# Kernel optimization log

Measured on AMD Instinct MI355X. Metric: run time of the kernel, lower is better.

The kernel has to match this reference:

```python
import jax, jax.numpy as jnp
import numpy as np

A_DIM = 6
VBR = jnp.array([300.0, 750.0, 1200.0, 1850.0, 2850.0, 4300.0])
MAX_BR = 4300.0
BUF = 30000.0  # buffer_size fixed to 30000 each forward
N_STEPS = 6    # unrolled iterations in the source (cooked_bw[0]..cooked_bw[5])


def _conv_feat(x, w, b):
    # 1-channel valid Conv1d(kernel=4) + ReLU, flattened channel-major like torch .view
    L = x.shape[0]
    idx = jnp.arange(L - 3)[:, None] + jnp.arange(4)[None, :]
    win = x[idx]                                   # (L-3, 4)
    out = jax.nn.relu(win @ w[:, 0, :].T + b)      # (L-3, 128)
    return out.T.reshape(-1)                       # (128*(L-3),)


def setup_inputs() -> dict:
    key = jax.random.key(0)
    ks = jax.random.split(key, 12)
    s = 0.1
    return {
        "inp": jax.random.uniform(ks[0], (8, 8), jnp.float32) + 0.1,
        "conv_w": jax.random.normal(ks[1], (128, 1, 4), jnp.float32) * s,
        "conv_b": jax.random.normal(ks[2], (128,), jnp.float32) * s,
        "w0": jax.random.normal(ks[3], (128, 1), jnp.float32) * s,
        "b0": jax.random.normal(ks[4], (128,), jnp.float32) * s,
        "w1": jax.random.normal(ks[5], (128, 1), jnp.float32) * s,
        "b1": jax.random.normal(ks[6], (128,), jnp.float32) * s,
        "w2": jax.random.normal(ks[7], (128, 1), jnp.float32) * s,
        "b2": jax.random.normal(ks[8], (128,), jnp.float32) * s,
        "w3": jax.random.normal(ks[9], (128, 2048), jnp.float32) * 0.02,
        "b3": jax.random.normal(ks[10], (128,), jnp.float32) * s,
        "w4": jax.random.normal(ks[11], (6, 128), jnp.float32) * s,
        "b4": jnp.zeros((6,), jnp.float32),
    }


def reference(inp, conv_w, conv_b, w0, b0, w1, b1, w2, b2, w3, b3, w4, b4):
    state = inp[:6, :]          # (6, 8)
    bw = inp[6, :]              # cooked bandwidth trace
    vs = inp[7, 0]              # base video chunk size
    vcs = vs * jnp.array([1.0, 2.0, 4.0, 8.0, 16.0, 32.0])  # video_chunk_sizes

    def net(st):
        s0 = jax.nn.relu(st[0, -1] * w0[:, 0] + b0)
        s1 = jax.nn.relu(st[1, -1] * w1[:, 0] + b1)
        s2 = _conv_feat(st[2, :], conv_w, conv_b)          # 640
        s3 = _conv_feat(st[3, :], conv_w, conv_b)          # 640
        s4 = _conv_feat(st[4, :A_DIM], conv_w, conv_b)     # 384
        s5 = st[4, -1] * w2[:, 0] + b2                     # no relu (matches source)
        feat = jnp.concatenate([s0, s1, s2, s3, s4, s5])   # (2048,)
        h = jax.nn.relu(w3 @ feat + b3)
        return w4 @ h + b4                                 # (6,)

    for i in range(N_STEPS):
        logits = net(state)
        a = jnp.argmax(logits)
        state = jnp.roll(state, -1, axis=1)
        delay = vcs[a] / bw[i] - BUF
        state = state.at[0, -1].set(VBR[a] / MAX_BR)
        state = state.at[1, -1].set(BUF / 1000.0 / 10.0)
        state = state.at[2, -1].set(vcs[a] / delay / 1000.0)
        state = state.at[3, -1].set(delay / 1000.0 / 10.0)
        state = state.at[4, :A_DIM].set(vcs / 1e6)
        state = state.at[5, -1].set((7.0 - i) / 8.0)

    return net(state)
```

## Files before the change

kernel.cpp:

```cpp
#include <hip/hip_runtime.h>

#define NBLK 32
#define OPB  4
#define TPB  256
#define FSTRIDE 32

__device__ __forceinline__ float relu_(float x) { return fmaxf(x, 0.f); }


__launch_bounds__(TPB, 1)
__global__ void actor_kernel(
    const float* __restrict__ inp,
    const float* __restrict__ conv_w, const float* __restrict__ conv_b,
    const float* __restrict__ w0, const float* __restrict__ b0,
    const float* __restrict__ w1, const float* __restrict__ b1,
    const float* __restrict__ w2, const float* __restrict__ b2,
    const float* __restrict__ w3, const float* __restrict__ b3,
    const float* __restrict__ w4, const float* __restrict__ b4,
    float* __restrict__ out, int* __restrict__ flags,
    float* __restrict__ partials)
{
    const int tid = threadIdx.x;
    const int b   = blockIdx.x;

    __shared__ __align__(16) float lw3[OPB * 2048];
    __shared__ __align__(16) float lfeat[2048];
    __shared__ __align__(16) float lcw[512];
    __shared__ float lcb[128];
    __shared__ float lw0[128], lb0[128], lw1[128], lb1[128], lw2v[128], lb2[128];
    __shared__ float lb3[128];
    __shared__ float lw4[768];
    __shared__ float lb4[8];
    __shared__ float st2[8], st3[8], st4[8];
    __shared__ float sx[8];
    __shared__ float lbw[8];
    __shared__ float h_lds[OPB];
    __shared__ float logits_l[8];

    {
        const float4* g = (const float4*)(w3 + b * OPB * 2048);
        float4* l = (float4*)lw3;
        #pragma unroll
        for (int idx = tid; idx < OPB * 2048 / 4; idx += TPB) l[idx] = g[idx];
    }
    for (int idx = tid; idx < 512; idx += TPB) lcw[idx] = conv_w[idx];
    if (tid < 128) {
        lcb[tid] = conv_b[tid];
        lw0[tid] = w0[tid];  lb0[tid] = b0[tid];
        lw1[tid] = w1[tid];  lb1[tid] = b1[tid];
        lw2v[tid] = w2[tid]; lb2[tid] = b2[tid];
        lb3[tid] = b3[tid];
    }
    for (int idx = tid; idx < 768; idx += TPB) lw4[idx] = w4[idx];
    if (tid < 6) lb4[tid] = b4[tid];
    if (tid < 8) {
        st2[tid] = inp[16 + tid];
        st3[tid] = inp[24 + tid];
        st4[tid] = inp[32 + tid];
        lbw[tid] = inp[48 + tid];
    }
    if (tid == 0) {
        sx[0] = inp[7];
        sx[1] = inp[15];
        sx[2] = inp[39];
        sx[3] = inp[32];
        sx[4] = inp[56];
    }
    __syncthreads();

    const int wv = tid >> 6, lane = tid & 63;

    for (int i = 0; i < 7; ++i) {
        if (tid < 128) {
            lfeat[tid]        = relu_(sx[0] * lw0[tid] + lb0[tid]);
            lfeat[1920 + tid] =        sx[2] * lw2v[tid] + lb2[tid];
        } else {
            int j = tid - 128;
            lfeat[128 + j] = relu_(sx[1] * lw1[j] + lb1[j]);
        }
        for (int m = tid; m < 640; m += TPB) {
            int c = m / 5, w = m - c * 5;
            float a2 = lcb[c], a3 = lcb[c];
            #pragma unroll
            for (int k = 0; k < 4; ++k) {
                float cw = lcw[c * 4 + k];
                a2 += st2[w + k] * cw;
                a3 += st3[w + k] * cw;
            }
            lfeat[256 + m] = relu_(a2);
            lfeat[896 + m] = relu_(a3);
        }
        for (int m = tid; m < 384; m += TPB) {
            int c = m / 3, w = m - c * 3;
            float a4 = lcb[c];
            #pragma unroll
            for (int k = 0; k < 4; ++k) a4 += st4[w + k] * lcw[c * 4 + k];
            lfeat[1536 + m] = relu_(a4);
        }
        __syncthreads();

        {
            const float4* wrow = (const float4*)(lw3 + wv * 2048);
            const float4* frow = (const float4*)lfeat;
            float4 acc = make_float4(0.f, 0.f, 0.f, 0.f);
            #pragma unroll
            for (int it = 0; it < 8; ++it) {
                float4 a = wrow[it * 64 + lane];
                float4 f = frow[it * 64 + lane];
                acc.x += a.x * f.x; acc.y += a.y * f.y;
                acc.z += a.z * f.z; acc.w += a.w * f.w;
            }
            float s = (acc.x + acc.y) + (acc.z + acc.w);
            #pragma unroll
            for (int off = 32; off > 0; off >>= 1) s += __shfl_xor(s, off);
            if (lane == 0) h_lds[wv] = relu_(s + lb3[b * OPB + wv]);
        }
        __syncthreads();

        if (tid < 6) {
            float p = 0.f;
            #pragma unroll
            for (int w = 0; w < OPB; ++w) p += lw4[tid * 128 + b * OPB + w] * h_lds[w];
            __hip_atomic_store(&partials[(i * NBLK + b) * 8 + tid], p,
                               __ATOMIC_RELAXED, __HIP_MEMORY_SCOPE_AGENT);
        }
        __syncthreads();
        if (tid == 0)
            __hip_atomic_store(&flags[b * FSTRIDE], i + 1,
                               __ATOMIC_RELEASE, __HIP_MEMORY_SCOPE_AGENT);

        if (i < 6 || b == 0) {
            if (tid < NBLK) {
                while (__hip_atomic_load(&flags[tid * FSTRIDE], __ATOMIC_ACQUIRE,
                                         __HIP_MEMORY_SCOPE_AGENT) < i + 1)
                    __builtin_amdgcn_s_sleep(1);
            }
        }
        __syncthreads();

        if (i < 6) {
            if (tid < 6) {
                float p = lb4[tid];
                #pragma unroll
                for (int bb = 0; bb < NBLK; ++bb)
                    p += __hip_atomic_load(&partials[(i * NBLK + bb) * 8 + tid],
                                           __ATOMIC_RELAXED, __HIP_MEMORY_SCOPE_AGENT);
                logits_l[tid] = p;
            }
            __syncthreads();
            if (tid == 0) {
                const float VBRc[6] = {300.f, 750.f, 1200.f, 1850.f, 2850.f, 4300.f};
                float best = logits_l[0]; int a = 0;
                #pragma unroll
                for (int r = 1; r < 6; ++r) {
                    float v = logits_l[r];
                    if (v > best) { best = v; a = r; }
                }
                float vs    = sx[4];
                float vca   = vs * (float)(1 << a);
                float delay = vca / lbw[i] - 30000.f;
                sx[0] = VBRc[a] * (1.f / 4300.f);
                sx[1] = 3.0f;
                #pragma unroll
                for (int c = 0; c < 7; ++c) { st2[c] = st2[c + 1]; st3[c] = st3[c + 1]; }
                st2[7] = vca / delay * 1e-3f;
                st3[7] = delay * 1e-4f;
                sx[2] = sx[3];
                sx[3] = vs * 1e-6f;
                #pragma unroll
                for (int j = 0; j < 6; ++j) st4[j] = vs * (float)(1 << j) * 1e-6f;
            }
            __syncthreads();
        } else if (b == 0) {
            if (tid < 6) {
                float p = lb4[tid];
                #pragma unroll
                for (int bb = 0; bb < NBLK; ++bb)
                    p += __hip_atomic_load(&partials[(6 * NBLK + bb) * 8 + tid],
                                           __ATOMIC_RELAXED, __HIP_MEMORY_SCOPE_AGENT);
                out[tid] = p;
            }
        }
    }
}

extern "C" void kernel_launch(void* const* d_in, const int* in_sizes, int n_in,
                              void* d_out, int out_size, void* d_ws, size_t ws_size,
                              hipStream_t stream) {
    const float* inp    = (const float*)d_in[0];
    const float* conv_w = (const float*)d_in[1];
    const float* conv_b = (const float*)d_in[2];
    const float* w0     = (const float*)d_in[3];
    const float* b0     = (const float*)d_in[4];
    const float* w1     = (const float*)d_in[5];
    const float* b1     = (const float*)d_in[6];
    const float* w2     = (const float*)d_in[7];
    const float* b2     = (const float*)d_in[8];
    const float* w3     = (const float*)d_in[9];
    const float* b3     = (const float*)d_in[10];
    const float* w4     = (const float*)d_in[11];
    const float* b4     = (const float*)d_in[12];

    int*   flags    = (int*)d_ws;
    float* partials = (float*)((char*)d_ws + 8192);

    actor_kernel<<<NBLK, TPB, 0, stream>>>(inp, conv_w, conv_b,
                                           w0, b0, w1, b1, w2, b2,
                                           w3, b3, w4, b4,
                                           (float*)d_out, flags, partials);
}
```

Baseline: 103.2 us.

## Speculatively evaluate all six next-step actions to halve grid-wide barrier count

Each iteration now computes step i's logits and, at the same time, all six candidate logits for step i+1, one per possible action a_i. The next state after an action differs only in a few features: the new last conv column of rows 2 and 3, s0, s1, s5 and the conv4 block. Per-action feature contributions are precomputed or split into shared and action-dependent parts. This cuts the cross-block flag barriers from 7 to 4, trading extra per-block arithmetic and 7x larger partial-sum traffic for fewer global synchronisation round trips.

```diff
diff --git a/kernel.cpp b/kernel.cpp
--- a/kernel.cpp
+++ b/kernel.cpp
@@ -1,9 +1,9 @@
 #include <hip/hip_runtime.h>
 
 #define NBLK 32
-#define OPB  4
 #define TPB  256
 #define FSTRIDE 32
+#define PSTRIDE 64
 
 __device__ __forceinline__ float relu_(float x) { return fmaxf(x, 0.f); }
 
@@ -23,36 +23,38 @@
     const int tid = threadIdx.x;
     const int b   = blockIdx.x;
 
-    __shared__ __align__(16) float lw3[OPB * 2048];
+    __shared__ __align__(16) float lw3[4 * 2048];
     __shared__ __align__(16) float lfeat[2048];
+    __shared__ __align__(16) float lc2[512], lc3[512];
+    __shared__ float lbase2[128], lbase3[128], ls5[128];
+    __shared__ float ls0[6 * 128];
+    __shared__ float ltmp[512];
     __shared__ __align__(16) float lcw[512];
     __shared__ float lcb[128];
-    __shared__ float lw0[128], lb0[128], lw1[128], lb1[128], lw2v[128], lb2[128];
-    __shared__ float lb3[128];
-    __shared__ float lw4[768];
-    __shared__ float lb4[8];
+    __shared__ float lw0v[128], lb0v[128], lw1v[128], lb1v[128];
+    __shared__ float lw2v[128], lb2v[128], lb3v[128];
+    __shared__ float lw4[768], lb4v[8];
     __shared__ float st2[8], st3[8], st4[8];
     __shared__ float sx[8];
     __shared__ float lbw[8];
-    __shared__ float h_lds[OPB];
-    __shared__ float logits_l[8];
+    __shared__ float h_lds[4], hv_lds[4 * 8];
+    __shared__ float red[48];
 
     {
-        const float4* g = (const float4*)(w3 + b * OPB * 2048);
-        float4* l = (float4*)lw3;
-        #pragma unroll
-        for (int idx = tid; idx < OPB * 2048 / 4; idx += TPB) l[idx] = g[idx];
+        const float4* g4 = (const float4*)(w3 + b * 4 * 2048);
+        float4* l4 = (float4*)lw3;
+        for (int idx = tid; idx < 2048; idx += TPB) l4[idx] = g4[idx];
     }
     for (int idx = tid; idx < 512; idx += TPB) lcw[idx] = conv_w[idx];
     if (tid < 128) {
-        lcb[tid] = conv_b[tid];
-        lw0[tid] = w0[tid];  lb0[tid] = b0[tid];
-        lw1[tid] = w1[tid];  lb1[tid] = b1[tid];
-        lw2v[tid] = w2[tid]; lb2[tid] = b2[tid];
-        lb3[tid] = b3[tid];
+        lcb[tid]  = conv_b[tid];
+        lw0v[tid] = w0[tid]; lb0v[tid] = b0[tid];
+        lw1v[tid] = w1[tid]; lb1v[tid] = b1[tid];
+        lw2v[tid] = w2[tid]; lb2v[tid] = b2[tid];
+        lb3v[tid] = b3[tid];
     }
     for (int idx = tid; idx < 768; idx += TPB) lw4[idx] = w4[idx];
-    if (tid < 6) lb4[tid] = b4[tid];
+    if (tid < 6) lb4v[tid] = b4[tid];
     if (tid < 8) {
         st2[tid] = inp[16 + tid];
         st3[tid] = inp[24 + tid];
@@ -60,23 +62,60 @@
         lbw[tid] = inp[48 + tid];
     }
     if (tid == 0) {
-        sx[0] = inp[7];
-        sx[1] = inp[15];
-        sx[2] = inp[39];
-        sx[3] = inp[32];
+        sx[0] = inp[7];   sx[1] = inp[15];
+        sx[2] = inp[39];  sx[3] = inp[32];
         sx[4] = inp[56];
     }
     __syncthreads();
 
+    if (tid < 128) {
+        const float vb[6] = {300.f, 750.f, 1200.f, 1850.f, 2850.f, 4300.f};
+        #pragma unroll
+        for (int v = 0; v < 6; ++v)
+            ls0[v * 128 + tid] = relu_(vb[v] * (1.f / 4300.f) * lw0v[tid] + lb0v[tid]);
+        ltmp[tid] = relu_(3.0f * lw1v[tid] + lb1v[tid]);
+    }
+    for (int m = tid; m < 384; m += TPB) {
+        int c = m / 3, w = m - c * 3;
+        float a = lcb[c];
+        #pragma unroll
+        for (int k = 0; k < 4; ++k)
+            a += sx[4] * (float)(1 << (w + k)) * 1e-6f * lcw[c * 4 + k];
+        ltmp[128 + m] = relu_(a);
+    }
+    __syncthreads();
+
     const int wv = tid >> 6, lane = tid & 63;
-
-    for (int i = 0; i < 7; ++i) {
+    const float* wr = lw3 + wv * 2048;
+    const float bias3 = lb3v[b * 4 + wv];
+
+    float hs0p[6], hs14p;
+    #pragma unroll
+    for (int v = 0; v < 6; ++v)
+        hs0p[v] = wr[lane] * ls0[v * 128 + lane] + wr[64 + lane] * ls0[v * 128 + 64 + lane];
+    hs14p = wr[128 + lane] * ltmp[lane] + wr[192 + lane] * ltmp[64 + lane];
+    #pragma unroll
+    for (int k = 0; k < 6; ++k) {
+        int m = lane + 64 * k;
+        hs14p += wr[1536 + m] * ltmp[128 + m];
+    }
+
+    const float VBRc[6] = {300.f, 750.f, 1200.f, 1850.f, 2850.f, 4300.f};
+
+    for (int g = 0; g < 3; ++g) {
+        const int i = 2 * g;
+
         if (tid < 128) {
-            lfeat[tid]        = relu_(sx[0] * lw0[tid] + lb0[tid]);
-            lfeat[1920 + tid] =        sx[2] * lw2v[tid] + lb2[tid];
+            lfeat[tid]        = relu_(sx[0] * lw0v[tid] + lb0v[tid]);
+            lfeat[1920 + tid] =        sx[2] * lw2v[tid] + lb2v[tid];
+            lbase2[tid] = st2[5] * lcw[tid*4] + st2[6] * lcw[tid*4+1]
+                        + st2[7] * lcw[tid*4+2] + lcb[tid];
+            lbase3[tid] = st3[5] * lcw[tid*4] + st3[6] * lcw[tid*4+1]
+                        + st3[7] * lcw[tid*4+2] + lcb[tid];
+            ls5[tid] = sx[3] * lw2v[tid] + lb2v[tid];
         } else {
             int j = tid - 128;
-            lfeat[128 + j] = relu_(sx[1] * lw1[j] + lb1[j]);
+            lfeat[128 + j] = relu_(sx[1] * lw1v[j] + lb1v[j]);
         }
         for (int m = tid; m < 640; m += TPB) {
             int c = m / 5, w = m - c * 5;
@@ -97,89 +136,227 @@
             for (int k = 0; k < 4; ++k) a4 += st4[w + k] * lcw[c * 4 + k];
             lfeat[1536 + m] = relu_(a4);
         }
-        __syncthreads();
-
+        for (int m = tid; m < 512; m += TPB) {
+            int c = m >> 2, w = m & 3;
+            float a2 = lcb[c], a3 = lcb[c];
+            #pragma unroll
+            for (int k = 0; k < 4; ++k) {
+                float cw = lcw[c * 4 + k];
+                a2 += st2[w + 1 + k] * cw;
+                a3 += st3[w + 1 + k] * cw;
+            }
+            lc2[m] = relu_(a2);
+            lc3[m] = relu_(a3);
+        }
+        __syncthreads();
+
+        float acc_i;
         {
-            const float4* wrow = (const float4*)(lw3 + wv * 2048);
-            const float4* frow = (const float4*)lfeat;
+            const float4* w4p = (const float4*)wr;
+            const float4* f4p = (const float4*)lfeat;
             float4 acc = make_float4(0.f, 0.f, 0.f, 0.f);
             #pragma unroll
             for (int it = 0; it < 8; ++it) {
-                float4 a = wrow[it * 64 + lane];
-                float4 f = frow[it * 64 + lane];
+                float4 a = w4p[it * 64 + lane];
+                float4 f = f4p[it * 64 + lane];
                 acc.x += a.x * f.x; acc.y += a.y * f.y;
                 acc.z += a.z * f.z; acc.w += a.w * f.w;
             }
-            float s = (acc.x + acc.y) + (acc.z + acc.w);
-            #pragma unroll
-            for (int off = 32; off > 0; off >>= 1) s += __shfl_xor(s, off);
-            if (lane == 0) h_lds[wv] = relu_(s + lb3[b * OPB + wv]);
-        }
-        __syncthreads();
-
-        if (tid < 6) {
+            acc_i = (acc.x + acc.y) + (acc.z + acc.w);
+        }
+
+        float acc_c = hs14p
+                    + wr[1920 + lane] * ls5[lane]
+                    + wr[1984 + lane] * ls5[64 + lane];
+        #pragma unroll
+        for (int k = 0; k < 8; ++k) {
+            int m = lane + 64 * k;
+            int col = 256 + (m >> 2) * 5 + (m & 3);
+            acc_c += wr[col] * lc2[m] + wr[640 + col] * lc3[m];
+        }
+
+        float n2[6], n3[6];
+        {
+            float bwi = lbw[i], vs = sx[4];
+            #pragma unroll
+            for (int v = 0; v < 6; ++v) {
+                float vca   = vs * (float)(1 << v);
+                float delay = vca / bwi - 30000.f;
+                n2[v] = vca / delay * 1e-3f;
+                n3[v] = delay * 1e-4f;
+            }
+        }
+        float accv[6];
+        #pragma unroll
+        for (int v = 0; v < 6; ++v) accv[v] = hs0p[v];
+        #pragma unroll
+        for (int t = 0; t < 2; ++t) {
+            int c = lane + 64 * t;
+            float cw3 = lcw[c * 4 + 3];
+            float bb2 = lbase2[c], bb3 = lbase3[c];
+            float wc2 = wr[256 + c * 5 + 4], wc3 = wr[896 + c * 5 + 4];
+            #pragma unroll
+            for (int v = 0; v < 6; ++v)
+                accv[v] += relu_(bb2 + n2[v] * cw3) * wc2
+                         + relu_(bb3 + n3[v] * cw3) * wc3;
+        }
+
+        #pragma unroll
+        for (int off = 32; off > 0; off >>= 1) {
+            acc_i += __shfl_xor(acc_i, off);
+            acc_c += __shfl_xor(acc_c, off);
+            #pragma unroll
+            for (int v = 0; v < 6; ++v) accv[v] += __shfl_xor(accv[v], off);
+        }
+        if (lane == 0) {
+            h_lds[wv] = relu_(acc_i + bias3);
+            #pragma unroll
+            for (int v = 0; v < 6; ++v)
+                hv_lds[wv * 8 + v] = relu_(acc_c + accv[v] + bias3);
+        }
+        __syncthreads();
+
+        if (tid < 42) {
+            int q = tid / 6, t = tid - q * 6;
             float p = 0.f;
-            #pragma unroll
-            for (int w = 0; w < OPB; ++w) p += lw4[tid * 128 + b * OPB + w] * h_lds[w];
-            __hip_atomic_store(&partials[(i * NBLK + b) * 8 + tid], p,
+            if (q == 0) {
+                #pragma unroll
+                for (int w = 0; w < 4; ++w) p += lw4[t * 128 + b * 4 + w] * h_lds[w];
+            } else {
+                #pragma unroll
+                for (int w = 0; w < 4; ++w) p += lw4[t * 128 + b * 4 + w] * hv_lds[w * 8 + (q - 1)];
+            }
+            __hip_atomic_store(&partials[(g * NBLK + b) * PSTRIDE + tid], p,
                                __ATOMIC_RELAXED, __HIP_MEMORY_SCOPE_AGENT);
         }
         __syncthreads();
         if (tid == 0)
-            __hip_atomic_store(&flags[b * FSTRIDE], i + 1,
+            __hip_atomic_store(&flags[b * FSTRIDE], g + 1,
                                __ATOMIC_RELEASE, __HIP_MEMORY_SCOPE_AGENT);
-
-        if (i < 6 || b == 0) {
-            if (tid < NBLK) {
-                while (__hip_atomic_load(&flags[tid * FSTRIDE], __ATOMIC_ACQUIRE,
-                                         __HIP_MEMORY_SCOPE_AGENT) < i + 1)
-                    __builtin_amdgcn_s_sleep(1);
-            }
-        }
-        __syncthreads();
-
-        if (i < 6) {
-            if (tid < 6) {
-                float p = lb4[tid];
-                #pragma unroll
-                for (int bb = 0; bb < NBLK; ++bb)
-                    p += __hip_atomic_load(&partials[(i * NBLK + bb) * 8 + tid],
-                                           __ATOMIC_RELAXED, __HIP_MEMORY_SCOPE_AGENT);
-                logits_l[tid] = p;
-            }
-            __syncthreads();
-            if (tid == 0) {
-                const float VBRc[6] = {300.f, 750.f, 1200.f, 1850.f, 2850.f, 4300.f};
-                float best = logits_l[0]; int a = 0;
-                #pragma unroll
-                for (int r = 1; r < 6; ++r) {
-                    float v = logits_l[r];
-                    if (v > best) { best = v; a = r; }
-                }
-                float vs    = sx[4];
-                float vca   = vs * (float)(1 << a);
+        if (tid < NBLK) {
+            while (__hip_atomic_load(&flags[tid * FSTRIDE], __ATOMIC_ACQUIRE,
+                                     __HIP_MEMORY_SCOPE_AGENT) < g + 1)
+                __builtin_amdgcn_s_sleep(1);
+        }
+        __syncthreads();
+
+        if (tid < 42) {
+            float p = lb4v[tid % 6];
+            #pragma unroll
+            for (int bb = 0; bb < NBLK; ++bb)
+                p += __hip_atomic_load(&partials[(g * NBLK + bb) * PSTRIDE + tid],
+                                       __ATOMIC_RELAXED, __HIP_MEMORY_SCOPE_AGENT);
+            red[tid] = p;
+        }
+        __syncthreads();
+        if (tid == 0) {
+            float best = red[0]; int a0 = 0;
+            #pragma unroll
+            for (int r = 1; r < 6; ++r) if (red[r] > best) { best = red[r]; a0 = r; }
+            best = red[6 + 6 * a0]; int a1 = 0;
+            #pragma unroll
+            for (int r = 1; r < 6; ++r)
+                if (red[6 + 6 * a0 + r] > best) { best = red[6 + 6 * a0 + r]; a1 = r; }
+
+            {
+                float vca = sx[4] * (float)(1 << a0);
                 float delay = vca / lbw[i] - 30000.f;
-                sx[0] = VBRc[a] * (1.f / 4300.f);
+                sx[0] = VBRc[a0] * (1.f / 4300.f);
                 sx[1] = 3.0f;
                 #pragma unroll
                 for (int c = 0; c < 7; ++c) { st2[c] = st2[c + 1]; st3[c] = st3[c + 1]; }
                 st2[7] = vca / delay * 1e-3f;
                 st3[7] = delay * 1e-4f;
-                sx[2] = sx[3];
-                sx[3] = vs * 1e-6f;
-                #pragma unroll
-                for (int j = 0; j < 6; ++j) st4[j] = vs * (float)(1 << j) * 1e-6f;
-            }
-            __syncthreads();
-        } else if (b == 0) {
-            if (tid < 6) {
-                float p = lb4[tid];
-                #pragma unroll
-                for (int bb = 0; bb < NBLK; ++bb)
-                    p += __hip_atomic_load(&partials[(6 * NBLK + bb) * 8 + tid],
-                                           __ATOMIC_RELAXED, __HIP_MEMORY_SCOPE_AGENT);
-                out[tid] = p;
-            }
+                sx[2] = sx[3]; sx[3] = sx[4] * 1e-6f;
+                #pragma unroll
+                for (int j = 0; j < 6; ++j) st4[j] = sx[4] * (float)(1 << j) * 1e-6f;
+            }
+            {
+                float vca = sx[4] * (float)(1 << a1);
+                float delay = vca / lbw[i + 1] - 30000.f;
+                sx[0] = VBRc[a1] * (1.f / 4300.f);
+                sx[1] = 3.0f;
+                #pragma unroll
+                for (int c = 0; c < 7; ++c) { st2[c] = st2[c + 1]; st3[c] = st3[c + 1]; }
+                st2[7] = vca / delay * 1e-3f;
+                st3[7] = delay * 1e-4f;
+                sx[2] = sx[3]; sx[3] = sx[4] * 1e-6f;
+                #pragma unroll
+                for (int j = 0; j < 6; ++j) st4[j] = sx[4] * (float)(1 << j) * 1e-6f;
+            }
+        }
+        __syncthreads();
+    }
+
+    if (tid < 128) {
+        lfeat[tid]        = relu_(sx[0] * lw0v[tid] + lb0v[tid]);
+        lfeat[1920 + tid] =        sx[2] * lw2v[tid] + lb2v[tid];
+    } else {
+        int j = tid - 128;
+        lfeat[128 + j] = relu_(sx[1] * lw1v[j] + lb1v[j]);
+    }
+    for (int m = tid; m < 640; m += TPB) {
+        int c = m / 5, w = m - c * 5;
+        float a2 = lcb[c], a3 = lcb[c];
+        #pragma unroll
+        for (int k = 0; k < 4; ++k) {
+            float cw = lcw[c * 4 + k];
+            a2 += st2[w + k] * cw;
+            a3 += st3[w + k] * cw;
+        }
+        lfeat[256 + m] = relu_(a2);
+        lfeat[896 + m] = relu_(a3);
+    }
+    for (int m = tid; m < 384; m += TPB) {
+        int c = m / 3, w = m - c * 3;
+        float a4 = lcb[c];
+        #pragma unroll
+        for (int k = 0; k < 4; ++k) a4 += st4[w + k] * lcw[c * 4 + k];
+        lfeat[1536 + m] = relu_(a4);
+    }
+    __syncthreads();
+    {
+        const float4* w4p = (const float4*)wr;
+        const float4* f4p = (const float4*)lfeat;
+        float4 acc = make_float4(0.f, 0.f, 0.f, 0.f);
+        #pragma unroll
+        for (int it = 0; it < 8; ++it) {
+            float4 a = w4p[it * 64 + lane];
+            float4 f = f4p[it * 64 + lane];
+            acc.x += a.x * f.x; acc.y += a.y * f.y;
+            acc.z += a.z * f.z; acc.w += a.w * f.w;
+        }
+        float s = (acc.x + acc.y) + (acc.z + acc.w);
+        #pragma unroll
+        for (int off = 32; off > 0; off >>= 1) s += __shfl_xor(s, off);
+        if (lane == 0) h_lds[wv] = relu_(s + bias3);
+    }
+    __syncthreads();
+    if (tid < 6) {
+        float p = 0.f;
+        #pragma unroll
+        for (int w = 0; w < 4; ++w) p += lw4[tid * 128 + b * 4 + w] * h_lds[w];
+        __hip_atomic_store(&partials[(3 * NBLK + b) * PSTRIDE + tid], p,
+                           __ATOMIC_RELAXED, __HIP_MEMORY_SCOPE_AGENT);
+    }
+    __syncthreads();
+    if (tid == 0)
+        __hip_atomic_store(&flags[b * FSTRIDE], 4,
+                           __ATOMIC_RELEASE, __HIP_MEMORY_SCOPE_AGENT);
+    if (b == 0) {
+        if (tid < NBLK) {
+            while (__hip_atomic_load(&flags[tid * FSTRIDE], __ATOMIC_ACQUIRE,
+                                     __HIP_MEMORY_SCOPE_AGENT) < 4)
+                __builtin_amdgcn_s_sleep(1);
+        }
+        __syncthreads();
+        if (tid < 6) {
+            float p = lb4v[tid];
+            #pragma unroll
+            for (int bb = 0; bb < NBLK; ++bb)
+                p += __hip_atomic_load(&partials[(3 * NBLK + bb) * PSTRIDE + tid],
+                                       __ATOMIC_RELAXED, __HIP_MEMORY_SCOPE_AGENT);
+            out[tid] = p;
         }
     }
 }
```

After: 99.95 us. 3.2% less time.
